# Performance work log

Hardware: AMD Instinct MI355X
Metric: run time of the kernel (lower is better)

The kernel has to match this reference:

```python
import jax, jax.numpy as jnp
import numpy as np
import math

N = 100000      # nodes
E = 1600000     # edges
D = 128         # embedding_size
H = 8           # num_heads
Dh = D // H     # head dim
F = 4 * D       # ffn hidden


def _layer_norm(x, g, b, eps=1e-5):
    mu = jnp.mean(x, axis=-1, keepdims=True)
    var = jnp.mean((x - mu) ** 2, axis=-1, keepdims=True)
    return (x - mu) * jax.lax.rsqrt(var + eps) * g + b


def setup_inputs() -> dict:
    key = jax.random.key(0)
    ks = jax.random.split(key, 12)
    s = 1.0 / math.sqrt(D)
    sf = 1.0 / math.sqrt(F)
    return {
        "feat": jax.random.normal(ks[0], (N, D), dtype=jnp.float32),
        "src": jax.random.randint(ks[1], (E,), 0, N, dtype=jnp.int32),
        "dst": jax.random.randint(ks[2], (E,), 0, N, dtype=jnp.int32),
        "Wq": jax.random.normal(ks[3], (D, D), dtype=jnp.float32) * s,
        "bq": jnp.zeros((D,), jnp.float32),
        "Wk": jax.random.normal(ks[4], (D, D), dtype=jnp.float32) * s,
        "bk": jnp.zeros((D,), jnp.float32),
        "Wv": jax.random.normal(ks[5], (D, D), dtype=jnp.float32) * s,
        "bv": jnp.zeros((D,), jnp.float32),
        "ln_g": jnp.ones((D,), jnp.float32),
        "ln_b": jnp.zeros((D,), jnp.float32),
        "W1": jax.random.normal(ks[6], (D, F), dtype=jnp.float32) * s,
        "b1": jnp.zeros((F,), jnp.float32),
        "alpha": jnp.full((F,), 0.25, jnp.float32),   # PReLU per-channel
        "W2": jax.random.normal(ks[7], (F, D), dtype=jnp.float32) * sf,
        "b2": jnp.zeros((D,), jnp.float32),
    }


def reference(feat, src, dst, Wq, bq, Wk, bk, Wv, bv, ln_g, ln_b, W1, b1, alpha, W2, b2):
    feat_c = jax.lax.stop_gradient(feat)  # feat_c = feat.detach()
    q = (feat @ Wq + bq).reshape(N, H, Dh)
    k = (feat_c @ Wk + bk).reshape(N, H, Dh)
    v = (feat_c @ Wv + bv).reshape(N, H, Dh)

    # u_dot_v: score per edge = <k[src], q[dst]> per head, scaled by sqrt(embedding_size)
    e = jnp.einsum('ehd,ehd->eh', k[src], q[dst]) / math.sqrt(D)  # [E, H]

    # edge_softmax over incoming edges of each destination node
    emax = jax.ops.segment_max(e, dst, num_segments=N)            # [N, H]
    ex = jnp.exp(e - emax[dst])                                   # [E, H]
    denom = jax.ops.segment_sum(ex, dst, num_segments=N)          # [N, H]
    a = ex / denom[dst]                                           # [E, H]

    # u_mul_e + sum: weighted scatter-aggregation into dst nodes
    m = v[src] * a[:, :, None]                                    # [E, H, Dh]
    rst = jax.ops.segment_sum(m, dst, num_segments=N)             # [N, H, Dh]
    rst = rst.reshape(N, D) + feat
    rst = _layer_norm(rst, ln_g, ln_b)

    # out_proj: Linear -> PReLU -> Linear (dropouts are identity at p=0)
    h = rst @ W1 + b1
    h = jnp.where(h > 0, h, alpha * h)
    ffn = h @ W2 + b2
    return _layer_norm(rst + ffn, ln_g, ln_b)  # original reuses ln1
```

## Files before the change

kernel.cpp:

```cpp
#include <hip/hip_runtime.h>
#include <hip/hip_bf16.h>

#define D 128
#define H 8
#define DH 16
#define FF 512
#define NBK 512
#define CHUNK 8192

typedef __hip_bfloat16 bf16;
typedef __attribute__((ext_vector_type(8))) short short8v;
typedef __attribute__((ext_vector_type(4))) float f32x4;

#define MFMA16(a, b, c) __builtin_amdgcn_mfma_f32_16x16x32_bf16((a), (b), (c), 0, 0, 0)

__device__ __forceinline__ unsigned short bfbits(float x) {
    bf16 h = __float2bfloat16(x);
    unsigned short s;
    __builtin_memcpy(&s, &h, 2);
    return s;
}

__device__ __forceinline__ void dec8(uint4 u, float* f) {
    f[0] = __uint_as_float(u.x << 16); f[1] = __uint_as_float(u.x & 0xffff0000u);
    f[2] = __uint_as_float(u.y << 16); f[3] = __uint_as_float(u.y & 0xffff0000u);
    f[4] = __uint_as_float(u.z << 16); f[5] = __uint_as_float(u.z & 0xffff0000u);
    f[6] = __uint_as_float(u.w << 16); f[7] = __uint_as_float(u.w & 0xffff0000u);
}

__global__ __launch_bounds__(256) void wsplit_all(
    const float* __restrict__ W1, const float* __restrict__ W2,
    const float* __restrict__ Wq, const float* __restrict__ Wk, const float* __restrict__ Wv,
    unsigned short* __restrict__ w1th, unsigned short* __restrict__ w1tl,
    unsigned short* __restrict__ w2th, unsigned short* __restrict__ w2tl,
    unsigned short* __restrict__ wqh,  unsigned short* __restrict__ wql,
    int* __restrict__ bcnt)
{
    const int y = blockIdx.y;
    const float* W;
    unsigned short *Th, *Tl;
    int K, logC;
    if (y == 0)      { W = W1; Th = w1th; Tl = w1tl; K = 128; logC = 9; }
    else if (y == 1) { W = W2; Th = w2th; Tl = w2tl; K = 512; logC = 7; }
    else {
        const int m = y - 2;
        W  = m == 0 ? Wq : (m == 1 ? Wk : Wv);
        Th = wqh + m * (D * D);
        Tl = wql + m * (D * D);
        K = 128; logC = 7;
    }
    if (y == 0 && blockIdx.x == 0)
        for (int j = threadIdx.x; j < NBK; j += 256) bcnt[j] = 0;

    int i = blockIdx.x * 256 + threadIdx.x;
    int total = K << logC;
    if (i >= total) return;
    int k = i >> logC;
    int n = i & ((1 << logC) - 1);
    float x = W[i];
    unsigned short hb = bfbits(x);
    float hf = __uint_as_float((unsigned)hb << 16);
    unsigned short lb = bfbits(x - hf);
    int NT = 1 << (logC - 4);
    int tile = (k >> 5) * NT + (n >> 4);
    int lane = ((k >> 3) & 3) * 16 + (n & 15);
    int idx = tile * 512 + lane * 8 + (k & 7);
    Th[idx] = hb;
    Tl[idx] = lb;
}

#define QXS 136

__global__ __launch_bounds__(256, 2) void qkv_mfma(
    const float* __restrict__ feat,
    const unsigned short* __restrict__ WTh, const unsigned short* __restrict__ WTl,
    const float* __restrict__ bq, const float* __restrict__ bk, const float* __restrict__ bv,
    bf16* __restrict__ q, bf16* __restrict__ k, bf16* __restrict__ v,
    int N)
{
    __shared__ unsigned short Xh[32 * QXS];
    __shared__ unsigned short Xl[32 * QXS];

    const int tid = threadIdx.x;
    const int n0 = blockIdx.x * 32;

    #pragma unroll
    for (int it = 0; it < 4; it++) {
        int idx = tid + it * 256;
        int row = idx >> 5;
        int part = idx & 31;
        float4 f = make_float4(0.f, 0.f, 0.f, 0.f);
        if (n0 + row < N) f = *(const float4*)(feat + (size_t)(n0 + row) * D + part * 4);
        const float xv[4] = {f.x, f.y, f.z, f.w};
        unsigned short hb[4], lb[4];
        #pragma unroll
        for (int j = 0; j < 4; j++) {
            hb[j] = bfbits(xv[j]);
            float hf = __uint_as_float((unsigned)hb[j] << 16);
            lb[j] = bfbits(xv[j] - hf);
        }
        uint2 ph, pl;
        ph.x = (unsigned)hb[0] | ((unsigned)hb[1] << 16);
        ph.y = (unsigned)hb[2] | ((unsigned)hb[3] << 16);
        pl.x = (unsigned)lb[0] | ((unsigned)lb[1] << 16);
        pl.y = (unsigned)lb[2] | ((unsigned)lb[3] << 16);
        *(uint2*)&Xh[row * QXS + part * 4] = ph;
        *(uint2*)&Xl[row * QXS + part * 4] = pl;
    }
    __syncthreads();

    const int w = tid >> 6, l = tid & 63;
    const int lr = l & 15;
    const int lg = l >> 4;

    f32x4 acc[2][6];
    const f32x4 zero4 = {0.f, 0.f, 0.f, 0.f};
    #pragma unroll
    for (int rt = 0; rt < 2; rt++)
        #pragma unroll
        for (int ct = 0; ct < 6; ct++) acc[rt][ct] = zero4;

    auto ldb = [&](int u, short8v* bh3, short8v* bl3) {
        const int ks = u >> 1, cb = (u & 1) * 3;
        #pragma unroll
        for (int j = 0; j < 3; j++) {
            const int g = w * 6 + cb + j;
            const size_t off = (size_t)(g >> 3) * 16384 +
                               (size_t)((ks * 8 + (g & 7)) * 512 + l * 8);
            bh3[j] = *(const short8v*)&WTh[off];
            bl3[j] = *(const short8v*)&WTl[off];
        }
    };

    short8v pbh[3][3], pbl[3][3];
    ldb(0, pbh[0], pbl[0]);
    ldb(1, pbh[1], pbl[1]);
    short8v ah0, ah1, al0, al1;

    #pragma unroll
    for (int u = 0; u < 8; u++) {
        if (u + 2 < 8) ldb(u + 2, pbh[(u + 2) % 3], pbl[(u + 2) % 3]);
        if ((u & 1) == 0) {
            const int k0 = (u >> 1) * 32;
            ah0 = *(const short8v*)&Xh[lr * QXS + k0 + lg * 8];
            ah1 = *(const short8v*)&Xh[(16 + lr) * QXS + k0 + lg * 8];
            al0 = *(const short8v*)&Xl[lr * QXS + k0 + lg * 8];
            al1 = *(const short8v*)&Xl[(16 + lr) * QXS + k0 + lg * 8];
        }
        const int cb = (u & 1) * 3;
        const short8v* bh = pbh[u % 3];
        const short8v* bl = pbl[u % 3];
        #pragma unroll
        for (int j = 0; j < 3; j++) acc[0][cb + j] = MFMA16(ah0, bh[j], acc[0][cb + j]);
        #pragma unroll
        for (int j = 0; j < 3; j++) acc[1][cb + j] = MFMA16(ah1, bh[j], acc[1][cb + j]);
        #pragma unroll
        for (int j = 0; j < 3; j++) acc[0][cb + j] = MFMA16(ah0, bl[j], acc[0][cb + j]);
        #pragma unroll
        for (int j = 0; j < 3; j++) acc[1][cb + j] = MFMA16(ah1, bl[j], acc[1][cb + j]);
        #pragma unroll
        for (int j = 0; j < 3; j++) acc[0][cb + j] = MFMA16(al0, bh[j], acc[0][cb + j]);
        #pragma unroll
        for (int j = 0; j < 3; j++) acc[1][cb + j] = MFMA16(al1, bh[j], acc[1][cb + j]);
    }

    #pragma unroll
    for (int ct = 0; ct < 6; ct++) {
        const int cbase = w * 96 + ct * 16;
        const int which = cbase >> 7;
        const int colin = (cbase & 127) + lr;
        const float* bias = which == 0 ? bq : (which == 1 ? bk : bv);
        bf16* outp       = which == 0 ? q  : (which == 1 ? k  : v);
        const float bb = bias[colin];
        #pragma unroll
        for (int rt = 0; rt < 2; rt++) {
            #pragma unroll
            for (int i = 0; i < 4; i++) {
                int row = n0 + rt * 16 + lg * 4 + i;
                if (row < N)
                    outp[(size_t)row * D + colin] = __float2bfloat16(acc[rt][ct][i] + bb);
            }
        }
    }
}

__global__ __launch_bounds__(256) void bucket_hist(
    const int* __restrict__ dst, int* __restrict__ bcnt, int E)
{
    __shared__ int bh[NBK];
    for (int j = threadIdx.x; j < NBK; j += 256) bh[j] = 0;
    __syncthreads();
    for (int i = blockIdx.x * 256 + threadIdx.x; i < E; i += gridDim.x * 256)
        atomicAdd(&bh[dst[i] >> 8], 1);
    __syncthreads();
    for (int j = threadIdx.x; j < NBK; j += 256)
        if (bh[j]) atomicAdd(&bcnt[j], bh[j]);
}

__global__ __launch_bounds__(256) void bucket_scan(
    const int* __restrict__ bcnt, int* __restrict__ bofsb, int* __restrict__ gcur)
{
    __shared__ int sA[NBK], sB[NBK];
    const int t = threadIdx.x;
    for (int j = t; j < NBK; j += 256) sA[j] = bcnt[j];
    __syncthreads();
    bool pb = false;
    for (int off = 1; off < NBK; off <<= 1) {
        const int* in = pb ? sB : sA;
        int* o        = pb ? sA : sB;
        for (int j = t; j < NBK; j += 256)
            o[j] = in[j] + (j >= off ? in[j - off] : 0);
        __syncthreads();
        pb = !pb;
    }
    const int* inc = pb ? sB : sA;
    for (int j = t; j < NBK; j += 256) {
        int ex = inc[j] - bcnt[j];
        bofsb[j] = ex;
        gcur[j]  = ex;
    }
}

__global__ __launch_bounds__(256) void binA(
    const int* __restrict__ src, const int* __restrict__ dst,
    int* __restrict__ gcur, unsigned* __restrict__ bpack, int E)
{
    __shared__ int hist[NBK], runc[NBK], gof[NBK];
    const int t = threadIdx.x;
    const int e0 = blockIdx.x * CHUNK;
    const int cnt = min(CHUNK, E - e0);

    for (int j = t; j < NBK; j += 256) { hist[j] = 0; runc[j] = 0; }
    __syncthreads();

    for (int i = t; i < cnt; i += 256)
        atomicAdd(&hist[dst[e0 + i] >> 8], 1);
    __syncthreads();

    for (int j = t; j < NBK; j += 256)
        if (hist[j] > 0) gof[j] = atomicAdd(&gcur[j], hist[j]);
    __syncthreads();

    for (int i = t; i < cnt; i += 256) {
        int d = dst[e0 + i];
        int s = src[e0 + i];
        int b = d >> 8;
        int r = atomicAdd(&runc[b], 1);
        bpack[gof[b] + r] = ((unsigned)(d & 255) << 24) | (unsigned)s;
    }
}

__global__ __launch_bounds__(256) void binB_fused(
    const unsigned* __restrict__ bpack, const int* __restrict__ bofsb,
    const int* __restrict__ bcnt,
    int* __restrict__ deg, int* __restrict__ row_off,
    int* __restrict__ csr, int N)
{
    __shared__ int dc[256];
    __shared__ int curl[256];
    __shared__ int wsum[4];
    const int t = threadIdx.x;
    const int b = blockIdx.x;
    const int bstart = bofsb[b], cnt = bcnt[b];

    dc[t] = 0;
    __syncthreads();
    for (int i = t; i < cnt; i += 256)
        atomicAdd(&dc[bpack[bstart + i] >> 24], 1);
    __syncthreads();

    const int myDeg = dc[t];
    int incl = myDeg;
    const int lane = t & 63;
    #pragma unroll
    for (int o = 1; o < 64; o <<= 1) {
        int nv = __shfl_up(incl, o);
        if (lane >= o) incl += nv;
    }
    if (lane == 63) wsum[t >> 6] = incl;
    __syncthreads();
    int woff = 0;
    #pragma unroll
    for (int kk = 0; kk < 4; kk++) if (kk < (t >> 6)) woff += wsum[kk];
    const int ex = bstart + woff + incl - myDeg;

    curl[t] = ex;
    const int node = b * 256 + t;
    if (node < N) { deg[node] = myDeg; row_off[node] = ex; }
    __syncthreads();

    for (int i = t; i < cnt; i += 256) {
        unsigned p = bpack[bstart + i];
        int pos = atomicAdd(&curl[p >> 24], 1);
        csr[pos] = (int)(p & 0xFFFFFFu);
    }
}

__global__ __launch_bounds__(64) void node_agg(
    const bf16* __restrict__ kb, const bf16* __restrict__ qb, const bf16* __restrict__ vb,
    const int* __restrict__ csr, const int* __restrict__ row_off, const int* __restrict__ deg,
    const float* __restrict__ feat, const float* __restrict__ g, const float* __restrict__ b,
    bf16* __restrict__ rst_ln, int N)
{
    __shared__ float qs[128];
    const int l = threadIdx.x;
    const int n = blockIdx.x;
    if (n >= N) return;

    unsigned qu = *(const unsigned*)(qb + (size_t)n * D + 2 * l);
    qs[2 * l]     = __uint_as_float(qu << 16);
    qs[2 * l + 1] = __uint_as_float(qu & 0xffff0000u);

    const int rs = row_off[n], dn = deg[n];
    const int el = l >> 3, h = l & 7, ha = l >> 3;

    float m = -3.0e38f, lsum = 0.f, acc0 = 0.f, acc1 = 0.f;

    if (dn > 0) {
        int sn = csr[rs + (el < dn ? el : 0)];
        const uint4* kp0 = (const uint4*)(kb + (size_t)sn * D + h * DH);
        uint4 k0 = kp0[0], k1 = kp0[1];

        for (int base = 0; base < dn; base += 8) {
            int sn_n = 0;
            uint4 kn0, kn1;
            const bool more = base + 8 < dn;
            if (more) {
                int ei = base + 8 + el;
                sn_n = csr[rs + (ei < dn ? ei : 0)];
                const uint4* kpn = (const uint4*)(kb + (size_t)sn_n * D + h * DH);
                kn0 = kpn[0]; kn1 = kpn[1];
            }

            const bool valid = base + el < dn;
            float kf[16];
            dec8(k0, kf); dec8(k1, kf + 8);
            const float* qp = &qs[h * DH];
            float s = 0.f;
            #pragma unroll
            for (int i = 0; i < 16; i++) s += kf[i] * qp[i];
            s *= 0.08838834764831845f;
            if (!valid) s = -3.0e38f;

            float cmax = s;
            cmax = fmaxf(cmax, __shfl_xor(cmax, 8));
            cmax = fmaxf(cmax, __shfl_xor(cmax, 16));
            cmax = fmaxf(cmax, __shfl_xor(cmax, 32));
            float m_new = fmaxf(m, cmax);
            float alphaH = __expf(m - m_new);
            float wgt = __expf(s - m_new);
            float wsum = wgt;
            wsum += __shfl_xor(wsum, 8);
            wsum += __shfl_xor(wsum, 16);
            wsum += __shfl_xor(wsum, 32);
            lsum = lsum * alphaH + wsum;
            m = m_new;

            float alphaA = __shfl(alphaH, ha);

            float na0 = 0.f, na1 = 0.f;
            #pragma unroll
            for (int e = 0; e < 8; e++) {
                int sne = __shfl(sn, e * 8);
                unsigned vu = *(const unsigned*)(vb + (size_t)sne * D + 2 * l);
                float wv = __shfl(wgt, e * 8 + ha);
                na0 += wv * __uint_as_float(vu << 16);
                na1 += wv * __uint_as_float(vu & 0xffff0000u);
            }
            acc0 = acc0 * alphaA + na0;
            acc1 = acc1 * alphaA + na1;

            if (more) { sn = sn_n; k0 = kn0; k1 = kn1; }
        }
    }

    float den = __shfl(lsum, ha);
    float v0 = (den > 0.f) ? acc0 / den : 0.f;
    float v1 = (den > 0.f) ? acc1 / den : 0.f;

    float2 fv = *(const float2*)(feat + (size_t)n * D + 2 * l);
    v0 += fv.x; v1 += fv.y;

    float s1 = v0 + v1, s2 = v0 * v0 + v1 * v1;
    #pragma unroll
    for (int o = 1; o < 64; o <<= 1) {
        s1 += __shfl_xor(s1, o);
        s2 += __shfl_xor(s2, o);
    }
    float mu = s1 * (1.f / 128.f);
    float var = s2 * (1.f / 128.f) - mu * mu;
    float rsq = rsqrtf(var + 1e-5f);
    float y0 = (v0 - mu) * rsq * g[2 * l]     + b[2 * l];
    float y1 = (v1 - mu) * rsq * g[2 * l + 1] + b[2 * l + 1];
    unsigned pk = (unsigned)bfbits(y0) | ((unsigned)bfbits(y1) << 16);
    *(unsigned*)(rst_ln + (size_t)n * D + 2 * l) = pk;
}

#define BM 32
#define XS 136
#define HS 520
#define YS 132

__global__ __launch_bounds__(256, 2) void ffn_mfma(
    const bf16* __restrict__ rst_ln,
    const unsigned short* __restrict__ W1Th, const unsigned short* __restrict__ W1Tl,
    const float* __restrict__ b1, const float* __restrict__ alpha,
    const unsigned short* __restrict__ W2Th, const unsigned short* __restrict__ W2Tl,
    const float* __restrict__ b2,
    const float* __restrict__ g, const float* __restrict__ bln,
    float* __restrict__ out, int N)
{
    __shared__ unsigned short Xs[BM * XS];
    __shared__ unsigned short HhBuf[BM * HS];
    __shared__ unsigned short Hl[BM * HS];

    const int tid = threadIdx.x;
    const int n0 = blockIdx.x * BM;

    #pragma unroll
    for (int it = 0; it < 2; it++) {
        int idx = tid + it * 256;
        int row = idx >> 4;
        int part = idx & 15;
        uint4 u = make_uint4(0u, 0u, 0u, 0u);
        if (n0 + row < N) u = *(const uint4*)(rst_ln + (size_t)(n0 + row) * D + part * 8);
        *(uint4*)&Xs[row * XS + part * 8] = u;
    }
    __syncthreads();

    const int w = tid >> 6, l = tid & 63;
    const int lr = l & 15;
    const int lg = l >> 4;

    const int colbase = w * 128;
    f32x4 acc1[2][8];
    const f32x4 zero4 = {0.f, 0.f, 0.f, 0.f};
    #pragma unroll
    for (int rt = 0; rt < 2; rt++)
        #pragma unroll
        for (int ct = 0; ct < 8; ct++) acc1[rt][ct] = zero4;

    auto ldb1 = [&](int u, short8v* bh4, short8v* bl4) {
        const int ks = u >> 1, cb = (u & 1) * 4;
        #pragma unroll
        for (int j = 0; j < 4; j++) {
            const size_t off = (size_t)((ks * 32 + w * 8 + cb + j) * 512 + l * 8);
            bh4[j] = *(const short8v*)&W1Th[off];
            bl4[j] = *(const short8v*)&W1Tl[off];
        }
    };

    {
        short8v pbh[3][4], pbl[3][4];
        ldb1(0, pbh[0], pbl[0]);
        ldb1(1, pbh[1], pbl[1]);
        short8v a0, a1;
        #pragma unroll
        for (int u = 0; u < 8; u++) {
            if (u + 2 < 8) ldb1(u + 2, pbh[(u + 2) % 3], pbl[(u + 2) % 3]);
            if ((u & 1) == 0) {
                const int k0 = (u >> 1) * 32;
                a0 = *(const short8v*)&Xs[lr * XS + k0 + lg * 8];
                a1 = *(const short8v*)&Xs[(16 + lr) * XS + k0 + lg * 8];
            }
            const int cb = (u & 1) * 4;
            const short8v* bh = pbh[u % 3];
            const short8v* bl = pbl[u % 3];
            #pragma unroll
            for (int j = 0; j < 4; j++) acc1[0][cb + j] = MFMA16(a0, bh[j], acc1[0][cb + j]);
            #pragma unroll
            for (int j = 0; j < 4; j++) acc1[1][cb + j] = MFMA16(a1, bh[j], acc1[1][cb + j]);
            #pragma unroll
            for (int j = 0; j < 4; j++) acc1[0][cb + j] = MFMA16(a0, bl[j], acc1[0][cb + j]);
            #pragma unroll
            for (int j = 0; j < 4; j++) acc1[1][cb + j] = MFMA16(a1, bl[j], acc1[1][cb + j]);
        }
    }

    #pragma unroll
    for (int ct = 0; ct < 8; ct++) {
        const int col = colbase + ct * 16 + lr;
        const float bb = b1[col];
        const float aa = alpha[col];
        #pragma unroll
        for (int rt = 0; rt < 2; rt++) {
            #pragma unroll
            for (int i = 0; i < 4; i++) {
                const int row = rt * 16 + lg * 4 + i;
                float hv = acc1[rt][ct][i] + bb;
                hv = hv > 0.f ? hv : aa * hv;
                unsigned short hb = bfbits(hv);
                float hf = __uint_as_float((unsigned)hb << 16);
                unsigned short lb = bfbits(hv - hf);
                HhBuf[row * HS + col] = hb;
                Hl[row * HS + col]    = lb;
            }
        }
    }
    __syncthreads();

    const int ob = w * 32;
    f32x4 acc2[2][2];
    #pragma unroll
    for (int rt = 0; rt < 2; rt++)
        #pragma unroll
        for (int ct = 0; ct < 2; ct++) acc2[rt][ct] = zero4;

    auto ldb2 = [&](int ks, short8v* bh2, short8v* bl2) {
        #pragma unroll
        for (int ct = 0; ct < 2; ct++) {
            const size_t off = (size_t)((ks * 8 + w * 2 + ct) * 512 + l * 8);
            bh2[ct] = *(const short8v*)&W2Th[off];
            bl2[ct] = *(const short8v*)&W2Tl[off];
        }
    };

    {
        short8v p2h[4][2], p2l[4][2];
        #pragma unroll
        for (int s = 0; s < 3; s++) ldb2(s, p2h[s], p2l[s]);
        #pragma unroll
        for (int ks = 0; ks < 16; ks++) {
            const int slot = ks & 3;
            if (ks + 3 < 16) ldb2(ks + 3, p2h[(ks + 3) & 3], p2l[(ks + 3) & 3]);
            const int k0 = ks * 32;
            short8v ah0 = *(const short8v*)&HhBuf[lr * HS + k0 + lg * 8];
            short8v ah1 = *(const short8v*)&HhBuf[(16 + lr) * HS + k0 + lg * 8];
            short8v al0 = *(const short8v*)&Hl[lr * HS + k0 + lg * 8];
            short8v al1 = *(const short8v*)&Hl[(16 + lr) * HS + k0 + lg * 8];
            const short8v* bh = p2h[slot];
            const short8v* bl = p2l[slot];
            acc2[0][0] = MFMA16(ah0, bh[0], acc2[0][0]);
            acc2[0][1] = MFMA16(ah0, bh[1], acc2[0][1]);
            acc2[1][0] = MFMA16(ah1, bh[0], acc2[1][0]);
            acc2[1][1] = MFMA16(ah1, bh[1], acc2[1][1]);
            acc2[0][0] = MFMA16(ah0, bl[0], acc2[0][0]);
            acc2[0][1] = MFMA16(ah0, bl[1], acc2[0][1]);
            acc2[1][0] = MFMA16(ah1, bl[0], acc2[1][0]);
            acc2[1][1] = MFMA16(ah1, bl[1], acc2[1][1]);
            acc2[0][0] = MFMA16(al0, bh[0], acc2[0][0]);
            acc2[0][1] = MFMA16(al0, bh[1], acc2[0][1]);
            acc2[1][0] = MFMA16(al1, bh[0], acc2[1][0]);
            acc2[1][1] = MFMA16(al1, bh[1], acc2[1][1]);
        }
    }
    __syncthreads();

    float* Yb = (float*)HhBuf;
    #pragma unroll
    for (int ct = 0; ct < 2; ct++) {
        const int col = ob + ct * 16 + lr;
        const float bb = b2[col];
        #pragma unroll
        for (int rt = 0; rt < 2; rt++) {
            #pragma unroll
            for (int i = 0; i < 4; i++) {
                const int row = rt * 16 + lg * 4 + i;
                float xr = __uint_as_float((unsigned)Xs[row * XS + col] << 16);
                Yb[row * YS + col] = acc2[rt][ct][i] + bb + xr;
            }
        }
    }
    __syncthreads();

    {
        const int row = tid >> 3;
        const int sub = tid & 7;
        const int c0 = sub * 16;
        const float* Yr = Yb + row * YS + c0;
        f32x4 v0 = *(const f32x4*)(Yr + 0);
        f32x4 v1 = *(const f32x4*)(Yr + 4);
        f32x4 v2 = *(const f32x4*)(Yr + 8);
        f32x4 v3 = *(const f32x4*)(Yr + 12);
        float s1 = 0.f, s2 = 0.f;
        #pragma unroll
        for (int c = 0; c < 4; c++) {
            s1 += v0[c] + v1[c] + v2[c] + v3[c];
            s2 += v0[c] * v0[c] + v1[c] * v1[c] + v2[c] * v2[c] + v3[c] * v3[c];
        }
        #pragma unroll
        for (int o = 1; o < 8; o <<= 1) {
            s1 += __shfl_xor(s1, o);
            s2 += __shfl_xor(s2, o);
        }
        float mu = s1 * (1.f / 128.f);
        float var = s2 * (1.f / 128.f) - mu * mu;
        float rs = rsqrtf(var + 1e-5f);
        const int gr = n0 + row;
        if (gr < N) {
            float* op = out + (size_t)gr * D + c0;
            f32x4 g0 = *(const f32x4*)(g + c0 + 0),  g1 = *(const f32x4*)(g + c0 + 4);
            f32x4 g2 = *(const f32x4*)(g + c0 + 8),  g3 = *(const f32x4*)(g + c0 + 12);
            f32x4 b0 = *(const f32x4*)(bln + c0 + 0), b1v = *(const f32x4*)(bln + c0 + 4);
            f32x4 b2v = *(const f32x4*)(bln + c0 + 8), b3 = *(const f32x4*)(bln + c0 + 12);
            *(f32x4*)(op + 0)  = (v0 - mu) * rs * g0 + b0;
            *(f32x4*)(op + 4)  = (v1 - mu) * rs * g1 + b1v;
            *(f32x4*)(op + 8)  = (v2 - mu) * rs * g2 + b2v;
            *(f32x4*)(op + 12) = (v3 - mu) * rs * g3 + b3;
        }
    }
}

extern "C" void kernel_launch(void* const* d_in, const int* in_sizes, int n_in,
                              void* d_out, int out_size, void* d_ws, size_t ws_size,
                              hipStream_t stream) {
    const float* feat = (const float*)d_in[0];
    const int*   src  = (const int*)d_in[1];
    const int*   dst  = (const int*)d_in[2];
    const float* Wq   = (const float*)d_in[3];
    const float* bq   = (const float*)d_in[4];
    const float* Wk   = (const float*)d_in[5];
    const float* bk   = (const float*)d_in[6];
    const float* Wv   = (const float*)d_in[7];
    const float* bv   = (const float*)d_in[8];
    const float* ln_g = (const float*)d_in[9];
    const float* ln_b = (const float*)d_in[10];
    const float* W1   = (const float*)d_in[11];
    const float* b1   = (const float*)d_in[12];
    const float* alp  = (const float*)d_in[13];
    const float* W2   = (const float*)d_in[14];
    const float* b2   = (const float*)d_in[15];
    float* out = (float*)d_out;

    const int N = in_sizes[0] / D;
    const int E = in_sizes[1];
    const int nbk = (N + 255) >> 8;

    char* p = (char*)d_ws;
    auto take = [&](size_t bytes) { char* r = p; p += (bytes + 255) & ~(size_t)255; return r; };
    bf16* qb    = (bf16*)take((size_t)N * D * 2);
    bf16* kb    = (bf16*)take((size_t)N * D * 2);
    bf16* vb    = (bf16*)take((size_t)N * D * 2);
    bf16* rstln = (bf16*)take((size_t)N * D * 2);
    int*  degb  = (int*)take((size_t)N * 4);
    int*  rowof = (int*)take((size_t)N * 4);
    int*  csr   = (int*)take((size_t)E * 4);
    unsigned* bpack = (unsigned*)take((size_t)E * 4);
    int*  bcnt  = (int*)take((size_t)NBK * 4);
    int*  bofsb = (int*)take((size_t)NBK * 4);
    int*  gcur  = (int*)take((size_t)NBK * 4);
    unsigned short* w1th = (unsigned short*)take((size_t)D * FF * 2);
    unsigned short* w1tl = (unsigned short*)take((size_t)D * FF * 2);
    unsigned short* w2th = (unsigned short*)take((size_t)D * FF * 2);
    unsigned short* w2tl = (unsigned short*)take((size_t)D * FF * 2);
    unsigned short* wqkvh = (unsigned short*)take((size_t)3 * D * D * 2);
    unsigned short* wqkvl = (unsigned short*)take((size_t)3 * D * D * 2);

    wsplit_all<<<dim3((D * FF + 255) / 256, 5), 256, 0, stream>>>(
        W1, W2, Wq, Wk, Wv, w1th, w1tl, w2th, w2tl, wqkvh, wqkvl, bcnt);

    qkv_mfma<<<(N + 31) / 32, 256, 0, stream>>>(
        feat, wqkvh, wqkvl, bq, bk, bv, qb, kb, vb, N);

    bucket_hist<<<256, 256, 0, stream>>>(dst, bcnt, E);
    bucket_scan<<<1, 256, 0, stream>>>(bcnt, bofsb, gcur);
    binA<<<(E + CHUNK - 1) / CHUNK, 256, 0, stream>>>(src, dst, gcur, bpack, E);
    binB_fused<<<nbk, 256, 0, stream>>>(bpack, bofsb, bcnt, degb, rowof, csr, N);

    node_agg<<<N, 64, 0, stream>>>(
        kb, qb, vb, csr, rowof, degb, feat, ln_g, ln_b, rstln, N);

    ffn_mfma<<<(N + BM - 1) / BM, 256, 0, stream>>>(
        rstln, w1th, w1tl, b1, alp, w2th, w2tl, b2, ln_g, ln_b, out, N);
}
```

Measured before the change: 468.5 us.

## Fuse bucket histogram and scan into QKV kernel; use bf16 dot2 in scores

Merges the edge-bucket histogram and its prefix scan into the QKV projection launch. Extra blocks build the histogram, and the last block to finish, detected through an atomic done-counter, runs the scan. This removes two kernel launches and lets the histogram run alongside the projection. Separately, the per-edge attention score in node_agg now uses the packed bf16 dot2 instruction on raw bf16 pairs instead of unpacking to fp32 and multiplying, which cuts ALU work. The cost is extra complexity in the last-block detection, which depends on correct fence ordering, and dot2 may round differently.

```diff
diff --git a/kernel.cpp b/kernel.cpp
--- a/kernel.cpp
+++ b/kernel.cpp
@@ -7,12 +7,26 @@
 #define FF 512
 #define NBK 512
 #define CHUNK 8192
+#define HISTB 256
 
 typedef __hip_bfloat16 bf16;
 typedef __attribute__((ext_vector_type(8))) short short8v;
 typedef __attribute__((ext_vector_type(4))) float f32x4;
 
 #define MFMA16(a, b, c) __builtin_amdgcn_mfma_f32_16x16x32_bf16((a), (b), (c), 0, 0, 0)
+
+#if defined(__has_builtin)
+#if __has_builtin(__builtin_amdgcn_fdot2_f32_bf16)
+#define USE_DOT2 1
+typedef __bf16 bf16x2v __attribute__((ext_vector_type(2)));
+__device__ __forceinline__ float dot2bf(unsigned a, unsigned b, float c) {
+    bf16x2v av, bv;
+    __builtin_memcpy(&av, &a, 4);
+    __builtin_memcpy(&bv, &b, 4);
+    return __builtin_amdgcn_fdot2_f32_bf16(av, bv, c, false);
+}
+#endif
+#endif
 
 __device__ __forceinline__ unsigned short bfbits(float x) {
     bf16 h = __float2bfloat16(x);
@@ -34,7 +48,7 @@
     unsigned short* __restrict__ w1th, unsigned short* __restrict__ w1tl,
     unsigned short* __restrict__ w2th, unsigned short* __restrict__ w2tl,
     unsigned short* __restrict__ wqh,  unsigned short* __restrict__ wql,
-    int* __restrict__ bcnt)
+    int* __restrict__ bcnt, int* __restrict__ donec)
 {
     const int y = blockIdx.y;
     const float* W;
@@ -49,8 +63,10 @@
         Tl = wql + m * (D * D);
         K = 128; logC = 7;
     }
-    if (y == 0 && blockIdx.x == 0)
+    if (y == 0 && blockIdx.x == 0) {
         for (int j = threadIdx.x; j < NBK; j += 256) bcnt[j] = 0;
+        if (threadIdx.x == 0) *donec = 0;
+    }
 
     int i = blockIdx.x * 256 + threadIdx.x;
     int total = K << logC;
@@ -71,18 +87,68 @@
 
 #define QXS 136
 
-__global__ __launch_bounds__(256, 2) void qkv_mfma(
+__global__ __launch_bounds__(256, 2) void qkv_hist(
     const float* __restrict__ feat,
     const unsigned short* __restrict__ WTh, const unsigned short* __restrict__ WTl,
     const float* __restrict__ bq, const float* __restrict__ bk, const float* __restrict__ bv,
     bf16* __restrict__ q, bf16* __restrict__ k, bf16* __restrict__ v,
-    int N)
+    int N,
+    const int* __restrict__ dst, int E,
+    int* __restrict__ bcnt, int* __restrict__ bofsb, int* __restrict__ gcur,
+    int* __restrict__ donec)
 {
     __shared__ unsigned short Xh[32 * QXS];
     __shared__ unsigned short Xl[32 * QXS];
+    __shared__ int lastFlag;
 
     const int tid = threadIdx.x;
-    const int n0 = blockIdx.x * 32;
+
+    if (blockIdx.x < HISTB) {
+        int* bh = (int*)Xh;
+        for (int j = tid; j < NBK; j += 256) bh[j] = 0;
+        __syncthreads();
+        for (int i = blockIdx.x * 256 + tid; i < E; i += HISTB * 256)
+            atomicAdd(&bh[dst[i] >> 8], 1);
+        __syncthreads();
+        for (int j = tid; j < NBK; j += 256)
+            if (bh[j]) atomicAdd(&bcnt[j], bh[j]);
+        __threadfence();
+        __syncthreads();
+        if (tid == 0) lastFlag = (atomicAdd(donec, 1) == HISTB - 1);
+        __syncthreads();
+        if (!lastFlag) return;
+
+        int* sA = (int*)Xh;
+        int* sB = (int*)Xl;
+        int myc[2];
+        #pragma unroll
+        for (int r = 0; r < 2; r++) {
+            int j = tid + r * 256;
+            myc[r] = atomicAdd(&bcnt[j], 0);
+            sA[j] = myc[r];
+        }
+        __syncthreads();
+        bool pb = false;
+        for (int off = 1; off < NBK; off <<= 1) {
+            const int* in = pb ? sB : sA;
+            int* o        = pb ? sA : sB;
+            for (int j = tid; j < NBK; j += 256)
+                o[j] = in[j] + (j >= off ? in[j - off] : 0);
+            __syncthreads();
+            pb = !pb;
+        }
+        const int* inc = pb ? sB : sA;
+        #pragma unroll
+        for (int r = 0; r < 2; r++) {
+            int j = tid + r * 256;
+            int ex = inc[j] - myc[r];
+            bofsb[j] = ex;
+            gcur[j]  = ex;
+        }
+        return;
+    }
+
+    const int n0 = (blockIdx.x - HISTB) * 32;
 
     #pragma unroll
     for (int it = 0; it < 4; it++) {
@@ -181,43 +247,6 @@
                     outp[(size_t)row * D + colin] = __float2bfloat16(acc[rt][ct][i] + bb);
             }
         }
-    }
-}
-
-__global__ __launch_bounds__(256) void bucket_hist(
-    const int* __restrict__ dst, int* __restrict__ bcnt, int E)
-{
-    __shared__ int bh[NBK];
-    for (int j = threadIdx.x; j < NBK; j += 256) bh[j] = 0;
-    __syncthreads();
-    for (int i = blockIdx.x * 256 + threadIdx.x; i < E; i += gridDim.x * 256)
-        atomicAdd(&bh[dst[i] >> 8], 1);
-    __syncthreads();
-    for (int j = threadIdx.x; j < NBK; j += 256)
-        if (bh[j]) atomicAdd(&bcnt[j], bh[j]);
-}
-
-__global__ __launch_bounds__(256) void bucket_scan(
-    const int* __restrict__ bcnt, int* __restrict__ bofsb, int* __restrict__ gcur)
-{
-    __shared__ int sA[NBK], sB[NBK];
-    const int t = threadIdx.x;
-    for (int j = t; j < NBK; j += 256) sA[j] = bcnt[j];
-    __syncthreads();
-    bool pb = false;
-    for (int off = 1; off < NBK; off <<= 1) {
-        const int* in = pb ? sB : sA;
-        int* o        = pb ? sA : sB;
-        for (int j = t; j < NBK; j += 256)
-            o[j] = in[j] + (j >= off ? in[j - off] : 0);
-        __syncthreads();
-        pb = !pb;
-    }
-    const int* inc = pb ? sB : sA;
-    for (int j = t; j < NBK; j += 256) {
-        int ex = inc[j] - bcnt[j];
-        bofsb[j] = ex;
-        gcur[j]  = ex;
     }
 }
 
@@ -302,17 +331,29 @@
     const float* __restrict__ feat, const float* __restrict__ g, const float* __restrict__ b,
     bf16* __restrict__ rst_ln, int N)
 {
-    __shared__ float qs[128];
     const int l = threadIdx.x;
     const int n = blockIdx.x;
     if (n >= N) return;
 
     unsigned qu = *(const unsigned*)(qb + (size_t)n * D + 2 * l);
+
+#ifdef USE_DOT2
+    __shared__ unsigned qsu[64];
+    qsu[l] = qu;
+#else
+    __shared__ float qs[128];
     qs[2 * l]     = __uint_as_float(qu << 16);
     qs[2 * l + 1] = __uint_as_float(qu & 0xffff0000u);
+#endif
 
     const int rs = row_off[n], dn = deg[n];
     const int el = l >> 3, h = l & 7, ha = l >> 3;
+
+#ifdef USE_DOT2
+    unsigned qreg[8];
+    #pragma unroll
+    for (int i = 0; i < 8; i++) qreg[i] = qsu[h * 8 + i];
+#endif
 
     float m = -3.0e38f, lsum = 0.f, acc0 = 0.f, acc1 = 0.f;
 
@@ -333,12 +374,22 @@
             }
 
             const bool valid = base + el < dn;
-            float kf[16];
-            dec8(k0, kf); dec8(k1, kf + 8);
-            const float* qp = &qs[h * DH];
             float s = 0.f;
-            #pragma unroll
-            for (int i = 0; i < 16; i++) s += kf[i] * qp[i];
+#ifdef USE_DOT2
+            {
+                const unsigned kp[8] = {k0.x, k0.y, k0.z, k0.w, k1.x, k1.y, k1.z, k1.w};
+                #pragma unroll
+                for (int i = 0; i < 8; i++) s = dot2bf(kp[i], qreg[i], s);
+            }
+#else
+            {
+                float kf[16];
+                dec8(k0, kf); dec8(k1, kf + 8);
+                const float* qp = &qs[h * DH];
+                #pragma unroll
+                for (int i = 0; i < 16; i++) s += kf[i] * qp[i];
+            }
+#endif
             s *= 0.08838834764831845f;
             if (!valid) s = -3.0e38f;
 
@@ -625,6 +676,7 @@
     const int N = in_sizes[0] / D;
     const int E = in_sizes[1];
     const int nbk = (N + 255) >> 8;
+    const int nQkv = (N + 31) / 32;
 
     char* p = (char*)d_ws;
     auto take = [&](size_t bytes) { char* r = p; p += (bytes + 255) & ~(size_t)255; return r; };
@@ -639,6 +691,7 @@
     int*  bcnt  = (int*)take((size_t)NBK * 4);
     int*  bofsb = (int*)take((size_t)NBK * 4);
     int*  gcur  = (int*)take((size_t)NBK * 4);
+    int*  donec = (int*)take(256);
     unsigned short* w1th = (unsigned short*)take((size_t)D * FF * 2);
     unsigned short* w1tl = (unsigned short*)take((size_t)D * FF * 2);
     unsigned short* w2th = (unsigned short*)take((size_t)D * FF * 2);
@@ -647,13 +700,12 @@
     unsigned short* wqkvl = (unsigned short*)take((size_t)3 * D * D * 2);
 
     wsplit_all<<<dim3((D * FF + 255) / 256, 5), 256, 0, stream>>>(
-        W1, W2, Wq, Wk, Wv, w1th, w1tl, w2th, w2tl, wqkvh, wqkvl, bcnt);
-
-    qkv_mfma<<<(N + 31) / 32, 256, 0, stream>>>(
-        feat, wqkvh, wqkvl, bq, bk, bv, qb, kb, vb, N);
-
-    bucket_hist<<<256, 256, 0, stream>>>(dst, bcnt, E);
-    bucket_scan<<<1, 256, 0, stream>>>(bcnt, bofsb, gcur);
+        W1, W2, Wq, Wk, Wv, w1th, w1tl, w2th, w2tl, wqkvh, wqkvl, bcnt, donec);
+
+    qkv_hist<<<HISTB + nQkv, 256, 0, stream>>>(
+        feat, wqkvh, wqkvl, bq, bk, bv, qb, kb, vb, N,
+        dst, E, bcnt, bofsb, gcur, donec);
+
     binA<<<(E + CHUNK - 1) / CHUNK, 256, 0, stream>>>(src, dst, gcur, bpack, E);
     binB_fused<<<nbk, 256, 0, stream>>>(bpack, bofsb, bcnt, degb, rowof, csr, N);
 
```

Result: slower. 480.9 us (+2.6%).
